# Optimization experiments

Measured on AMD Instinct MI355X. Metric: run time of the kernel, lower is better.

The kernel has to match this reference:

```python
import jax, jax.numpy as jnp
import numpy as np

RADIUS = 5
KERNEL = 2 * RADIUS + 1  # 11
N_PATCHES = KERNEL * KERNEL  # 121
SIGMA_DIAG = np.array([10.0, 10.0, 0.02, 0.02, 0.02, 0.1, 0.1, 0.1], dtype=np.float32)


def _shift(x):
    # x: [B, C, H, W] -> [B, P, C, H, W] with P = KERNEL^2 reflect-padded window shifts
    b, c, h, w = x.shape
    xp = jnp.pad(x, ((0, 0), (0, 0), (RADIUS, RADIUS), (RADIUS, RADIUS)), mode='reflect')
    patches = [xp[:, :, dy:dy + h, dx:dx + w]
               for dy in range(KERNEL) for dx in range(KERNEL)]
    return jnp.stack(patches, axis=1)


def setup_inputs() -> dict:
    key = jax.random.key(0)
    k1, k2 = jax.random.split(key)
    image = jax.random.uniform(k1, (2, 3, 256, 256), dtype=jnp.float32)
    guidance = jax.random.uniform(k2, (2, 8, 256, 256), dtype=jnp.float32)
    return {"image": image, "guidance": guidance}


def reference(image, guidance):
    # sigma_inv = inverse of diag(SIGMA_DIAG): diagonal, so just reciprocal per channel
    sigma_inv = jnp.asarray(1.0 / SIGMA_DIAG, dtype=guidance.dtype)  # [8]

    sg = _shift(guidance)                       # [B, P, 8, H, W]
    center = sg[:, N_PATCHES // 2:N_PATCHES // 2 + 1]
    diff = sg - center                          # [B, P, 8, H, W]
    # Mahalanobis^2 with diagonal sigma_inv: sum_c diff^2 / sigma_c
    maha_sq = jnp.einsum('bpchw,c->bphw', diff * diff, sigma_inv)
    weights = jnp.exp(-0.5 * maha_sq)           # [B, P, H, W]

    si = _shift(image)                          # [B, P, 3, H, W]
    weighted_sum = jnp.einsum('bpchw,bphw->bchw', si, weights)
    sum_w = jnp.clip(jnp.sum(weights, axis=1, keepdims=False), 1e-10, None)  # [B, H, W]
    return weighted_sum / sum_w[:, None]        # [B, 3, H, W]
```

## Files before the change

### kernel.cpp

```cpp
#include <hip/hip_runtime.h>

#define RADIUS 5
#define KSIZE  11
#define TXN    16
#define TYN    16
#define TILEX  32
#define TILEY  16
#define HX     (TILEX + 2*RADIUS)
#define HY     (TILEY + 2*RADIUS)
#define HPITCH 21
#define H      256
#define W      256

#define COEF_A (-0.072134752f)
#define COEF_B (-36.06737602f)
#define COEF_C (-7.213475204f)

__device__ __forceinline__ float wcalc(const float4 a, const float4 g,
                                       const float4 cA, const float4 cB) {
    const float d0 = a.x - cA.x, d1 = a.y - cA.y;
    const float d2 = a.z - cA.z, d3 = a.w - cA.w;
    const float d4 = g.x - cB.x, d5 = g.y - cB.y;
    const float d6 = g.z - cB.z, d7 = g.w - cB.w;
    const float sA = d0 * d0 + d1 * d1;
    const float sB = d2 * d2 + d3 * d3 + d4 * d4;
    const float sC = d5 * d5 + d6 * d6 + d7 * d7;
    return __builtin_amdgcn_exp2f(COEF_A * sA + COEF_B * sB + COEF_C * sC);
}

__global__ __launch_bounds__(256, 1) void jbf_kernel(
    const float* __restrict__ image,
    const float* __restrict__ guidance,
    float* __restrict__ out)
{
    __shared__ float4 g0e[HY * HPITCH], g0o[HY * HPITCH];
    __shared__ float4 g1e[HY * HPITCH], g1o[HY * HPITCH];
    __shared__ float4 ime[HY * HPITCH], imo[HY * HPITCH];

    const int b       = blockIdx.z;
    const int tile_x0 = blockIdx.x * TILEX;
    const int tile_y0 = blockIdx.y * TILEY;
    const int tid     = threadIdx.y * TXN + threadIdx.x;

    const float* gbase = guidance + (size_t)b * 8 * H * W;
    const float* ibase = image    + (size_t)b * 3 * H * W;

    for (int idx = tid; idx < HX * HY; idx += TXN * TYN) {
        const int ly = idx / HX;
        const int lx = idx - ly * HX;
        int gy = tile_y0 - RADIUS + ly;
        int gx = tile_x0 - RADIUS + lx;
        gy = (gy < 0) ? -gy : ((gy >= H) ? 2 * (H - 1) - gy : gy);
        gx = (gx < 0) ? -gx : ((gx >= W) ? 2 * (W - 1) - gx : gx);
        const int off = gy * W + gx;
        const int l   = ly * HPITCH + (lx >> 1);
        const float4 v0 = make_float4(gbase[0*H*W+off], gbase[1*H*W+off],
                                      gbase[2*H*W+off], gbase[3*H*W+off]);
        const float4 v1 = make_float4(gbase[4*H*W+off], gbase[5*H*W+off],
                                      gbase[6*H*W+off], gbase[7*H*W+off]);
        const float4 vi = make_float4(ibase[0*H*W+off], ibase[1*H*W+off],
                                      ibase[2*H*W+off], 0.f);
        if (lx & 1) { g0o[l] = v0; g1o[l] = v1; imo[l] = vi; }
        else        { g0e[l] = v0; g1e[l] = v1; ime[l] = vi; }
    }
    __syncthreads();

    const int tx = threadIdx.x;
    const int ty = threadIdx.y;

    const int crow = (ty + RADIUS) * HPITCH;
    const float4 c0A = g0o[crow + tx + 2], c0B = g1o[crow + tx + 2];
    const float4 c1A = g0e[crow + tx + 3], c1B = g1e[crow + tx + 3];

    float a00 = 0.f, a01 = 0.f, a02 = 0.f, sw0 = 0.f;
    float a10 = 0.f, a11 = 0.f, a12 = 0.f, sw1 = 0.f;

    for (int dy = 0; dy < KSIZE; ++dy) {
        const int rb = (ty + dy) * HPITCH + tx;
        #pragma unroll
        for (int k = 0; k <= 5; ++k) {
            const float4 Eg0 = g0e[rb + k], Eg1 = g1e[rb + k], Eim = ime[rb + k];
            const float4 Og0 = g0o[rb + k], Og1 = g1o[rb + k], Oim = imo[rb + k];

            {
                const float w = wcalc(Eg0, Eg1, c0A, c0B);
                sw0 += w; a00 += w * Eim.x; a01 += w * Eim.y; a02 += w * Eim.z;
            }
            if (k <= 4) {
                const float w = wcalc(Og0, Og1, c0A, c0B);
                sw0 += w; a00 += w * Oim.x; a01 += w * Oim.y; a02 += w * Oim.z;
            }
            {
                const float w = wcalc(Og0, Og1, c1A, c1B);
                sw1 += w; a10 += w * Oim.x; a11 += w * Oim.y; a12 += w * Oim.z;
            }
            if (k >= 1) {
                const float w = wcalc(Eg0, Eg1, c1A, c1B);
                sw1 += w; a10 += w * Eim.x; a11 += w * Eim.y; a12 += w * Eim.z;
            }
        }
    }

    const float inv0 = 1.0f / sw0;
    const float inv1 = 1.0f / sw1;
    const size_t o = (size_t)b * 3 * H * W + (size_t)(tile_y0 + ty) * W
                   + (size_t)(tile_x0 + 2 * tx);
    float2* __restrict__ o2 = (float2*)(out + o);
    o2[0]             = make_float2(a00 * inv0, a10 * inv1);
    o2[(H*W) / 2]     = make_float2(a01 * inv0, a11 * inv1);
    o2[(2*H*W) / 2]   = make_float2(a02 * inv0, a12 * inv1);
}

extern "C" void kernel_launch(void* const* d_in, const int* in_sizes, int n_in,
                              void* d_out, int out_size, void* d_ws, size_t ws_size,
                              hipStream_t stream) {
    const float* image    = (const float*)d_in[0];
    const float* guidance = (const float*)d_in[1];
    float* out            = (float*)d_out;

    const int B = in_sizes[0] / (3 * H * W);
    dim3 grid(W / TILEX, H / TILEY, B);
    dim3 block(TXN, TYN);
    hipLaunchKernelGGL(jbf_kernel, grid, block, 0, stream, image, guidance, out);
}
```

Before: 75.46 us.

## Split window rows across thread pairs and reduce partial sums with shuffles

Each block now has 512 threads. Every output pixel pair is handled by two lanes: one takes the even window rows and the other the odd rows, and their partial sums are combined with __shfl_xor before one lane writes the result. This doubles the thread count per block to raise occupancy and latency hiding on a grid of only 256 blocks. The cost is some imbalance (6 rows vs 5 rows per lane), eight shuffles per pixel, and half the lanes sitting idle during the write.

```diff
diff --git a/kernel.cpp b/kernel.cpp
--- a/kernel.cpp
+++ b/kernel.cpp
@@ -2,8 +2,6 @@
 
 #define RADIUS 5
 #define KSIZE  11
-#define TXN    16
-#define TYN    16
 #define TILEX  32
 #define TILEY  16
 #define HX     (TILEX + 2*RADIUS)
@@ -28,7 +26,7 @@
     return __builtin_amdgcn_exp2f(COEF_A * sA + COEF_B * sB + COEF_C * sC);
 }
 
-__global__ __launch_bounds__(256, 1) void jbf_kernel(
+__global__ __launch_bounds__(512, 2) void jbf_kernel(
     const float* __restrict__ image,
     const float* __restrict__ guidance,
     float* __restrict__ out)
@@ -40,12 +38,15 @@
     const int b       = blockIdx.z;
     const int tile_x0 = blockIdx.x * TILEX;
     const int tile_y0 = blockIdx.y * TILEY;
-    const int tid     = threadIdx.y * TXN + threadIdx.x;
+    const int half    = threadIdx.x;
+    const int txp     = threadIdx.y;
+    const int typ     = threadIdx.z;
+    const int tid     = (typ * 16 + txp) * 2 + half;
 
     const float* gbase = guidance + (size_t)b * 8 * H * W;
     const float* ibase = image    + (size_t)b * 3 * H * W;
 
-    for (int idx = tid; idx < HX * HY; idx += TXN * TYN) {
+    for (int idx = tid; idx < HX * HY; idx += 512) {
         const int ly = idx / HX;
         const int lx = idx - ly * HX;
         int gy = tile_y0 - RADIUS + ly;
@@ -65,50 +66,61 @@
     }
     __syncthreads();
 
-    const int tx = threadIdx.x;
-    const int ty = threadIdx.y;
-
-    const int crow = (ty + RADIUS) * HPITCH;
-    const float4 c0A = g0o[crow + tx + 2], c0B = g1o[crow + tx + 2];
-    const float4 c1A = g0e[crow + tx + 3], c1B = g1e[crow + tx + 3];
+    const int crow = (typ + RADIUS) * HPITCH;
+    const float4 c0A = g0o[crow + txp + 2], c0B = g1o[crow + txp + 2];
+    const float4 c1A = g0e[crow + txp + 3], c1B = g1e[crow + txp + 3];
 
     float a00 = 0.f, a01 = 0.f, a02 = 0.f, sw0 = 0.f;
     float a10 = 0.f, a11 = 0.f, a12 = 0.f, sw1 = 0.f;
 
-    for (int dy = 0; dy < KSIZE; ++dy) {
-        const int rb = (ty + dy) * HPITCH + tx;
-        #pragma unroll
-        for (int k = 0; k <= 5; ++k) {
-            const float4 Eg0 = g0e[rb + k], Eg1 = g1e[rb + k], Eim = ime[rb + k];
-            const float4 Og0 = g0o[rb + k], Og1 = g1o[rb + k], Oim = imo[rb + k];
+    for (int i = 0; i < 6; ++i) {
+        const int dy = 2 * i + half;
+        if (dy < KSIZE) {
+            const int rb = (typ + dy) * HPITCH + txp;
+            #pragma unroll
+            for (int k = 0; k <= 5; ++k) {
+                const float4 Eg0 = g0e[rb + k], Eg1 = g1e[rb + k], Eim = ime[rb + k];
+                const float4 Og0 = g0o[rb + k], Og1 = g1o[rb + k], Oim = imo[rb + k];
 
-            {
-                const float w = wcalc(Eg0, Eg1, c0A, c0B);
-                sw0 += w; a00 += w * Eim.x; a01 += w * Eim.y; a02 += w * Eim.z;
-            }
-            if (k <= 4) {
-                const float w = wcalc(Og0, Og1, c0A, c0B);
-                sw0 += w; a00 += w * Oim.x; a01 += w * Oim.y; a02 += w * Oim.z;
-            }
-            {
-                const float w = wcalc(Og0, Og1, c1A, c1B);
-                sw1 += w; a10 += w * Oim.x; a11 += w * Oim.y; a12 += w * Oim.z;
-            }
-            if (k >= 1) {
-                const float w = wcalc(Eg0, Eg1, c1A, c1B);
-                sw1 += w; a10 += w * Eim.x; a11 += w * Eim.y; a12 += w * Eim.z;
+                {
+                    const float w = wcalc(Eg0, Eg1, c0A, c0B);
+                    sw0 += w; a00 += w * Eim.x; a01 += w * Eim.y; a02 += w * Eim.z;
+                }
+                if (k <= 4) {
+                    const float w = wcalc(Og0, Og1, c0A, c0B);
+                    sw0 += w; a00 += w * Oim.x; a01 += w * Oim.y; a02 += w * Oim.z;
+                }
+                {
+                    const float w = wcalc(Og0, Og1, c1A, c1B);
+                    sw1 += w; a10 += w * Oim.x; a11 += w * Oim.y; a12 += w * Oim.z;
+                }
+                if (k >= 1) {
+                    const float w = wcalc(Eg0, Eg1, c1A, c1B);
+                    sw1 += w; a10 += w * Eim.x; a11 += w * Eim.y; a12 += w * Eim.z;
+                }
             }
         }
     }
 
-    const float inv0 = 1.0f / sw0;
-    const float inv1 = 1.0f / sw1;
-    const size_t o = (size_t)b * 3 * H * W + (size_t)(tile_y0 + ty) * W
-                   + (size_t)(tile_x0 + 2 * tx);
-    float2* __restrict__ o2 = (float2*)(out + o);
-    o2[0]             = make_float2(a00 * inv0, a10 * inv1);
-    o2[(H*W) / 2]     = make_float2(a01 * inv0, a11 * inv1);
-    o2[(2*H*W) / 2]   = make_float2(a02 * inv0, a12 * inv1);
+    sw0 += __shfl_xor(sw0, 1);
+    a00 += __shfl_xor(a00, 1);
+    a01 += __shfl_xor(a01, 1);
+    a02 += __shfl_xor(a02, 1);
+    sw1 += __shfl_xor(sw1, 1);
+    a10 += __shfl_xor(a10, 1);
+    a11 += __shfl_xor(a11, 1);
+    a12 += __shfl_xor(a12, 1);
+
+    if (half == 0) {
+        const float inv0 = 1.0f / sw0;
+        const float inv1 = 1.0f / sw1;
+        const size_t o = (size_t)b * 3 * H * W + (size_t)(tile_y0 + typ) * W
+                       + (size_t)(tile_x0 + 2 * txp);
+        float2* __restrict__ o2 = (float2*)(out + o);
+        o2[0]           = make_float2(a00 * inv0, a10 * inv1);
+        o2[(H*W) / 2]   = make_float2(a01 * inv0, a11 * inv1);
+        o2[(2*H*W) / 2] = make_float2(a02 * inv0, a12 * inv1);
+    }
 }
 
 extern "C" void kernel_launch(void* const* d_in, const int* in_sizes, int n_in,
@@ -120,6 +132,6 @@
 
     const int B = in_sizes[0] / (3 * H * W);
     dim3 grid(W / TILEX, H / TILEY, B);
-    dim3 block(TXN, TYN);
+    dim3 block(2, 16, 16);
     hipLaunchKernelGGL(jbf_kernel, grid, block, 0, stream, image, guidance, out);
 }
```

Result: faster. 73.76 us (-2.3%).
